# Optimization experiments

Hardware: AMD Instinct MI355X
Metric: run time of the kernel (lower is better)

## Reference

```python
import jax, jax.numpy as jnp
import numpy as np

H = 256   # hidden_size
D = 256   # embedding_dim
C = 111   # num_classes


def _pos_encoding(L, d):
    pos = jnp.arange(L, dtype=jnp.float32)[:, None]
    div = jnp.exp(jnp.arange(0, d, 2, dtype=jnp.float32) * (-np.log(10000.0) / d))
    pe = jnp.zeros((L, d), dtype=jnp.float32)
    pe = pe.at[:, 0::2].set(jnp.sin(pos * div))
    pe = pe.at[:, 1::2].set(jnp.cos(pos * div))
    return pe


def setup_inputs() -> dict:
    key = jax.random.key(0)
    ks = jax.random.split(key, 12)
    B, Cin, Hh, Ww, T = 64, 1024, 16, 64, 64
    s = 0.02
    return {
        "feature_map": jax.random.normal(ks[0], (B, Cin, Hh, Ww), jnp.float32),
        "count_vector": jax.random.uniform(ks[1], (B, C), jnp.float32),
        "target": jax.random.randint(ks[2], (B, T), 0, C),
        "conv_w": jax.random.normal(ks[3], (2 * H, Cin), jnp.float32) * s,
        "conv_b": jnp.zeros((2 * H,), jnp.float32),
        "emb": jax.random.normal(ks[4], (C, D), jnp.float32) * s,
        "gru_wih": jax.random.normal(ks[5], (3 * H, D + H + C), jnp.float32) * s,
        "gru_whh": jax.random.normal(ks[6], (3 * H, H), jnp.float32) * s,
        "gru_bih": jnp.zeros((3 * H,), jnp.float32),
        "gru_bhh": jnp.zeros((3 * H,), jnp.float32),
        "attn_w": jax.random.normal(ks[7], (H, 2 * H), jnp.float32) * s,
        "attn_b": jnp.zeros((H,), jnp.float32),
        "attn_v": jax.random.normal(ks[8], (1, H), jnp.float32) * s,
        "attn_vb": jnp.zeros((1,), jnp.float32),
        "cov_w": jax.random.normal(ks[9], (H, 1), jnp.float32) * s,
        "cov_b": jnp.zeros((H,), jnp.float32),
        "out_w": jax.random.normal(ks[10], (C, 2 * H + C), jnp.float32) * s,
        "out_b": jnp.zeros((C,), jnp.float32),
    }


def reference(feature_map, count_vector, target, conv_w, conv_b, emb,
              gru_wih, gru_whh, gru_bih, gru_bhh, attn_w, attn_b,
              attn_v, attn_vb, cov_w, cov_b, out_w, out_b):
    B, _, hh, ww = feature_map.shape
    L = hh * ww
    # 1x1 conv + permute to (B, h, w, 2H), add positional encoding, flatten
    feats = jnp.einsum('bchw,oc->bhwo', feature_map, conv_w) + conv_b
    pe = _pos_encoding(L, 2 * H).reshape(hh, ww, 2 * H)
    feats = (feats + pe[None]).reshape(B, L, 2 * H)
    # attention_w(projected_features) is time-invariant -> hoist out of the loop
    Wf = jnp.einsum('bld,hd->blh', feats, attn_w) + attn_b  # (B, L, H)

    # teacher forcing with ratio 1.0: inputs are <sos>=1 then target[:, :-1]
    y_in = jnp.concatenate([jnp.ones((B, 1), target.dtype), target[:, :-1]], axis=1)

    def gru_cell(x, h):  # PyTorch GRUCell math
        gi = x @ gru_wih.T + gru_bih
        gh = h @ gru_whh.T + gru_bhh
        i_r, i_z, i_n = jnp.split(gi, 3, axis=-1)
        h_r, h_z, h_n = jnp.split(gh, 3, axis=-1)
        r = jax.nn.sigmoid(i_r + h_r)
        z = jax.nn.sigmoid(i_z + h_z)
        n = jnp.tanh(i_n + r * h_n)
        return (1.0 - z) * n + z * h

    def step(carry, y_t):
        h, cov = carry  # h: (B,H), cov: (B,L)
        embedded = emb[y_t]
        a = jnp.tanh(Wf + cov[:, :, None] * cov_w[:, 0] + cov_b + h[:, None, :])
        scores = jnp.einsum('blh,h->bl', a, attn_v[0]) + attn_vb[0]
        alpha = jax.nn.softmax(scores, axis=1)
        cov = cov + alpha
        context = jnp.einsum('bl,bld->bd', alpha, feats)[:, :H]
        x = jnp.concatenate([embedded, context, count_vector], axis=1)
        h = gru_cell(x, h)
        out_t = jnp.concatenate([h, context, count_vector], axis=1) @ out_w.T + out_b
        return (h, cov), out_t

    h0 = jnp.zeros((B, H), feats.dtype)
    cov0 = jnp.zeros((B, L), feats.dtype)
    _, outs = jax.lax.scan(step, (h0, cov0), y_in.T)  # (T, B, C)
    return jnp.transpose(outs, (1, 0, 2))
```

## Files before the change

### kernel.cpp

```cpp
#include <hip/hip_runtime.h>
#include <hip/hip_bf16.h>
#include <cstdint>
#include <cstddef>

#define B_   64
#define CIN  1024
#define L_   1024
#define T_   64
#define Hh_  256
#define Dd_  256
#define Cc_  111
#define NO_  512
#define KX_  623

typedef __attribute__((ext_vector_type(8))) short short8;
typedef __attribute__((ext_vector_type(4))) float floatx4;

__device__ __forceinline__ float bf2f(unsigned short u) {
    union { unsigned int i; float f; } v; v.i = ((unsigned int)u) << 16; return v.f;
}
__device__ __forceinline__ unsigned short f2bf(float f) {
    union { float f; unsigned int i; } v; v.f = f;
    return (unsigned short)((v.i + 0x7fffu + ((v.i >> 16) & 1u)) >> 16);
}
__device__ __forceinline__ float frcp(float x) { return __builtin_amdgcn_rcpf(x); }
__device__ __forceinline__ float tanh_fast(float x) {
    return 1.0f - 2.0f * frcp(1.0f + __expf(2.0f * x));
}
__device__ __forceinline__ float sig_fast(float x) {
    return frcp(1.0f + __expf(-x));
}


__global__ void pe_kernel(float* __restrict__ PE) {
    int idx = blockIdx.x * 256 + threadIdx.x;
    if (idx >= L_ * NO_) return;
    int l = idx >> 9, j = idx & 511;
    int i2 = j & ~1;
    float div = expf((float)i2 * (-9.210340371976184f / 512.0f));
    float arg = (float)l * div;
    PE[idx] = (j & 1) ? cosf(arg) : sinf(arg);
}

__global__ void wc_kernel(const float* __restrict__ conv_w,
                          const float* __restrict__ attn_w,
                          unsigned short* __restrict__ Wc) {
    int c = blockIdx.x * 256 + threadIdx.x;
    int o = blockIdx.y;
    float v;
    if (o < 256) {
        v = conv_w[(size_t)o * CIN + c];
    } else {
        const float* aw = attn_w + (size_t)(o - 256) * 512;
        float a = 0.0f;
        for (int d = 0; d < 512; ++d)
            a = fmaf(aw[d], conv_w[(size_t)d * CIN + c], a);
        v = a;
    }
    Wc[(size_t)o * CIN + c] = f2bf(v);
}

__global__ void biasf_kernel(const float* __restrict__ conv_b,
                             const float* __restrict__ PE,
                             float* __restrict__ biasC) {
    int idx = blockIdx.x * 256 + threadIdx.x;
    int l = idx >> 8, j = idx & 255;
    biasC[(size_t)l * NO_ + j] = conv_b[j] + PE[(size_t)l * NO_ + j];
}

__global__ void biasw_kernel(const float* __restrict__ conv_b,
                             const float* __restrict__ PE,
                             const float* __restrict__ attn_w,
                             const float* __restrict__ attn_b,
                             float* __restrict__ biasC) {
    int l = blockIdx.x * 256 + threadIdx.x;
    int h = blockIdx.y;
    const float* aw = attn_w + (size_t)h * 512;
    const float* pe = PE + (size_t)l * NO_;
    float a = 0.0f;
    for (int d = 0; d < 512; ++d)
        a = fmaf(aw[d], conv_b[d] + pe[d], a);
    biasC[(size_t)l * NO_ + 256 + h] = a + attn_b[h];
}

__global__ void wiht_kernel(const float* __restrict__ wih, unsigned short* __restrict__ WihT) {
    int idx = blockIdx.x * 256 + threadIdx.x;
    if (idx >= 768 * KX_) return;
    int o = idx / KX_, k = idx - o * KX_;
    WihT[(size_t)k * 768 + o] = f2bf(wih[idx]);
}
__global__ void whht_kernel(const float* __restrict__ whh, unsigned short* __restrict__ WhhT) {
    int idx = blockIdx.x * 256 + threadIdx.x;
    if (idx >= 768 * 256) return;
    int o = idx >> 8, k = idx & 255;
    WhhT[(size_t)k * 768 + o] = f2bf(whh[idx]);
}
__global__ void woutt_kernel(const float* __restrict__ outw, unsigned short* __restrict__ WoutT) {
    int idx = blockIdx.x * 256 + threadIdx.x;
    if (idx >= Cc_ * KX_) return;
    int c = idx / KX_, k = idx - c * KX_;
    WoutT[(size_t)k * 128 + c] = f2bf(outw[idx]);
}

__global__ void zero_kernel(int* __restrict__ p, int n) {
    int i = blockIdx.x * 256 + threadIdx.x;
    if (i < n) p[i] = 0;
}

__global__ __launch_bounds__(256) void gemm_feats(
    const float* __restrict__ fm,
    const unsigned short* __restrict__ Wc,
    const float* __restrict__ biasC,
    unsigned short* __restrict__ F) {
    __shared__ __align__(16) unsigned short Als[128 * 40];
    __shared__ __align__(16) unsigned short Bls[128 * 40];
    const int tid  = threadIdx.x;
    const int bx   = blockIdx.x;
    const int bb   = bx >> 3;
    const int l0   = (bx & 7) << 7;
    const int n0   = blockIdx.y << 7;
    const int wid  = tid >> 6;
    const int lane = tid & 63;
    const int m0w  = (wid & 1) << 6;
    const int n0w  = (wid >> 1) << 6;
    const int quad = lane >> 4;
    const int l16  = lane & 15;

    floatx4 acc[4][4];
#pragma unroll
    for (int i = 0; i < 4; ++i)
#pragma unroll
        for (int j = 0; j < 4; ++j)
            acc[i][j] = (floatx4){0.f, 0.f, 0.f, 0.f};

    const int lt    = tid & 127;
    const int chalf = tid >> 7;
    const float* fmb = fm + ((size_t)bb * CIN) * L_ + l0 + lt;
    const int bo = tid >> 2;
    const int bc = (tid & 3) << 3;
    const int swzA = ((lt >> 2) & 3) << 3;

    for (int kk = 0; kk < 32; ++kk) {
        const int c0 = kk << 5;
        __syncthreads();
#pragma unroll
        for (int i = 0; i < 8; ++i) {
            int cc = (chalf + (i << 1)) << 1;
            float v0 = fmb[(size_t)(c0 + cc) * L_];
            float v1 = fmb[(size_t)(c0 + cc + 1) * L_];
            unsigned int pk = (unsigned int)f2bf(v0) | ((unsigned int)f2bf(v1) << 16);
            *(unsigned int*)(&Als[lt * 40 + (cc ^ swzA)]) = pk;
        }
#pragma unroll
        for (int i = 0; i < 2; ++i) {
            int o = bo + (i << 6);
            uint4 w = *(const uint4*)(&Wc[(size_t)(n0 + o) * CIN + c0 + bc]);
            *(uint4*)(&Bls[o * 40 + bc]) = w;
        }
        __syncthreads();
        short8 afr[4], bfr[4];
#pragma unroll
        for (int mf = 0; mf < 4; ++mf) {
            int mm = m0w + (mf << 4) + l16;
            int k0 = (quad << 3) ^ (((mm >> 2) & 3) << 3);
            afr[mf] = *(const short8*)(&Als[mm * 40 + k0]);
        }
#pragma unroll
        for (int nf = 0; nf < 4; ++nf) {
            int nn = n0w + (nf << 4) + l16;
            bfr[nf] = *(const short8*)(&Bls[nn * 40 + (quad << 3)]);
        }
#pragma unroll
        for (int mf = 0; mf < 4; ++mf)
#pragma unroll
            for (int nf = 0; nf < 4; ++nf)
                acc[mf][nf] = __builtin_amdgcn_mfma_f32_16x16x32_bf16(afr[mf], bfr[nf], acc[mf][nf], 0, 0, 0);
    }

#pragma unroll
    for (int mf = 0; mf < 4; ++mf) {
#pragma unroll
        for (int nf = 0; nf < 4; ++nf) {
            int colg = n0 + n0w + (nf << 4) + l16;
#pragma unroll
            for (int r = 0; r < 4; ++r) {
                int lb = l0 + m0w + (mf << 4) + (quad << 2) + r;
                float v = acc[mf][nf][r] + biasC[(size_t)lb * NO_ + colg];
                F[((size_t)bb * L_ + lb) * NO_ + colg] = f2bf(v);
            }
        }
    }
}


__device__ __forceinline__ void batch_barrier(int* bar, int target, int tid) {
    __syncthreads();
    if (tid == 0) {
        __hip_atomic_fetch_add(bar, 1, __ATOMIC_RELEASE, __HIP_MEMORY_SCOPE_AGENT);
        while (__hip_atomic_load(bar, __ATOMIC_RELAXED, __HIP_MEMORY_SCOPE_AGENT) < target) {
            __builtin_amdgcn_s_sleep(2);
        }
    }
    __syncthreads();
}

__global__ __launch_bounds__(1024, 4) void decoder_kernel(
    const unsigned short* __restrict__ F,
    const unsigned short* __restrict__ WihT,
    const unsigned short* __restrict__ WhhT,
    const unsigned short* __restrict__ WoutT,
    const float* __restrict__ cvv,
    const int* __restrict__ tgt,
    const float* __restrict__ emb,
    const float* __restrict__ bih,
    const float* __restrict__ bhh,
    const float* __restrict__ attn_v,
    const float* __restrict__ attn_vb,
    const float* __restrict__ cov_w,
    const float* __restrict__ cov_b,
    const float* __restrict__ outb,
    int* __restrict__ bar,
    float* __restrict__ gsum,
    float* __restrict__ gctx,
    float* __restrict__ ggih,
    float* __restrict__ OUT) {
    __shared__ __align__(16) unsigned short Wls[256 * 256];
    __shared__ float sc[256];
    __shared__ float cov[256];
    __shared__ float xv[640];
    __shared__ float xo[640];
    __shared__ float hv[256];
    __shared__ __align__(16) float hbs[256];
    __shared__ __align__(16) float cwls[256];
    __shared__ __align__(16) float avls[256];
    __shared__ float gi[768];
    __shared__ float gh[768];
    __shared__ float ctxp[2048];
    __shared__ float outp[1024];
    __shared__ float red[32];
    __shared__ int   tok[T_];

    const int tid  = threadIdx.x;
    const int bxr  = blockIdx.x;
    const int q_   = bxr >> 3;
    const int sub  = q_ & 3;
    const int b    = (bxr & 7) | ((q_ >> 2) << 3);
    const int l0   = sub << 8;
    const int lane = tid & 63;
    const int wid  = tid >> 6;
    const int l16  = tid & 15;
    const int lg   = tid >> 4;

    int* mybar = bar + b * 16;

    if (tid < 256) {
        cov[tid] = 0.0f; hv[tid] = 0.0f; hbs[tid] = cov_b[tid];
        cwls[tid] = cov_w[tid]; avls[tid] = attn_v[tid];
    }
    if (tid >= 512 && tid < 512 + Cc_) xv[tid] = cvv[b * Cc_ + (tid - 512)];
    if (tid >= KX_ && tid < 640) xo[tid] = 0.0f;
    if (tid < T_) tok[tid] = (tid == 0) ? 1 : tgt[b * T_ + tid - 1];

    const float avb = attn_vb[0];

#pragma unroll
    for (int i = 0; i < 8; ++i) {
        int c   = (i << 10) + tid;
        int row = c >> 5;
        int col = (c & 31) << 3;
        *(uint4*)(&Wls[(row << 8) + col]) =
            *(const uint4*)(F + (((size_t)(b * L_ + l0 + row)) << 9) + Hh_ + col);
    }

    unsigned int fctx[32];
    {
        const int hp = (tid & 127) << 1;
        const int ch = tid >> 7;
        const unsigned short* fb = F + (((size_t)(b * L_ + l0 + (ch << 5))) << 9) + hp;
#pragma unroll
        for (int i = 0; i < 32; ++i)
            fctx[i] = *(const unsigned int*)(fb + ((size_t)i << 9));
    }

    const int cbase = sub * 28;
    const int ccnt  = (sub == 3) ? 27 : 28;
    const int kg0 = sub * 156;
    const int kg1 = (kg0 + 156 > KX_) ? KX_ : kg0 + 156;
    const int kh0 = sub << 6;

    unsigned short wout_r[20];
    {
        int cc = tid & 31, ch = tid >> 5, k0 = ch * 20;
#pragma unroll
        for (int i = 0; i < 20; ++i) {
            int k = k0 + i;
            wout_r[i] = (k < KX_) ? WoutT[(size_t)k * 128 + cbase + cc] : (unsigned short)0;
        }
    }

    int nsync = 0;
    __syncthreads();

    float ecur = 0.0f;
    if (tid < 256) ecur = emb[(size_t)tok[0] * Dd_ + tid];

    for (int t = 0; t < T_; ++t) {
        const int par = t & 1;
        float* myctx = gctx + (((size_t)b * 2 + par) * 4) * 256;
        float* mysum = gsum + ((size_t)b * 2 + par) * 4;
        float* mygg  = ggih + (((size_t)b * 2 + par) * 4) * 1536;

        if (tid < 256) {
            xv[tid] = ecur;
            if (t + 1 < T_) ecur = emb[(size_t)tok[t + 1] * Dd_ + tid];
        }

#pragma unroll
        for (int pass = 0; pass < 4; ++pass) {
            int ll = (pass << 6) + lg;
            float covl = cov[ll];
            const unsigned short* wf = &Wls[ll << 8];
            float a = 0.0f;
#pragma unroll
            for (int j = 0; j < 4; ++j) {
                const int hb0 = (j << 6) + (l16 << 2);
                uint2 w = *(const uint2*)(wf + hb0);
                float4 cw4 = *(const float4*)(&cwls[hb0]);
                float4 av4 = *(const float4*)(&avls[hb0]);
                float4 hb4 = *(const float4*)(&hbs[hb0]);
                float g0 = bf2f((unsigned short)(w.x & 0xffffu)) + fmaf(covl, cw4.x, hb4.x);
                float g1 = bf2f((unsigned short)(w.x >> 16))     + fmaf(covl, cw4.y, hb4.y);
                float g2 = bf2f((unsigned short)(w.y & 0xffffu)) + fmaf(covl, cw4.z, hb4.z);
                float g3 = bf2f((unsigned short)(w.y >> 16))     + fmaf(covl, cw4.w, hb4.w);
                a = fmaf(av4.x, tanh_fast(g0), a);
                a = fmaf(av4.y, tanh_fast(g1), a);
                a = fmaf(av4.z, tanh_fast(g2), a);
                a = fmaf(av4.w, tanh_fast(g3), a);
            }
            a += __shfl_xor(a, 1);
            a += __shfl_xor(a, 2);
            a += __shfl_xor(a, 4);
            a += __shfl_xor(a, 8);
            if (l16 == 0) sc[ll] = __expf(a + avb);
        }
        __syncthreads();

        if (tid < 256) {
            float e = sc[tid];
#pragma unroll
            for (int off = 1; off < 64; off <<= 1) e += __shfl_xor(e, off);
            if (lane == 0) red[wid] = e;
        }

        {
            int hp = (tid & 127) << 1;
            int ch = tid >> 7;
            float c0a = 0.0f, c1a = 0.0f;
#pragma unroll
            for (int i = 0; i < 32; ++i) {
                float al = sc[(ch << 5) + i];
                unsigned int w = fctx[i];
                c0a = fmaf(al, bf2f((unsigned short)(w & 0xffffu)), c0a);
                c1a = fmaf(al, bf2f((unsigned short)(w >> 16)), c1a);
            }
            ctxp[(ch << 8) + hp]     = c0a;
            ctxp[(ch << 8) + hp + 1] = c1a;
        }
        __syncthreads();

        if (tid < 256) {
            float s2 = 0.0f;
#pragma unroll
            for (int i = 0; i < 8; ++i) s2 += ctxp[(i << 8) + tid];
            __hip_atomic_store(&myctx[sub * 256 + tid], s2, __ATOMIC_RELAXED, __HIP_MEMORY_SCOPE_AGENT);
        } else if (tid == 256) {
            float ss = red[0] + red[1] + red[2] + red[3];
            __hip_atomic_store(&mysum[sub], ss, __ATOMIC_RELAXED, __HIP_MEMORY_SCOPE_AGENT);
        }

        ++nsync;
        batch_barrier(mybar, 4 * nsync, tid);

        float s2 = 0.0f;
        if (tid < 256) {
#pragma unroll
            for (int s = 0; s < 4; ++s)
                s2 += __hip_atomic_load(&myctx[s * 256 + tid], __ATOMIC_RELAXED, __HIP_MEMORY_SCOPE_AGENT);
        } else if (tid == 256) {
            float S = 0.0f;
#pragma unroll
            for (int s = 0; s < 4; ++s)
                S += __hip_atomic_load(&mysum[s], __ATOMIC_RELAXED, __HIP_MEMORY_SCOPE_AGENT);
            red[16] = frcp(S);
        }
        __syncthreads();
        float rS = red[16];
        if (tid < 256) {
            xv[256 + tid] = s2 * rS;
            cov[tid] += sc[tid] * rS;
        }
        __syncthreads();

        if (tid < 384) {
            int o = tid << 1;
            float a0 = 0.0f, a1 = 0.0f;
            const unsigned short* wp = WihT + (size_t)kg0 * 768 + o;
#pragma unroll 4
            for (int k = kg0; k < kg1; ++k) {
                float x = xv[k];
                unsigned int w = *(const unsigned int*)wp;
                wp += 768;
                a0 = fmaf(x, bf2f((unsigned short)(w & 0xffffu)), a0);
                a1 = fmaf(x, bf2f((unsigned short)(w >> 16)), a1);
            }
            __hip_atomic_store(&mygg[sub * 1536 + o],     a0, __ATOMIC_RELAXED, __HIP_MEMORY_SCOPE_AGENT);
            __hip_atomic_store(&mygg[sub * 1536 + o + 1], a1, __ATOMIC_RELAXED, __HIP_MEMORY_SCOPE_AGENT);
        } else if (tid < 768) {
            int o = (tid - 384) << 1;
            float a0 = 0.0f, a1 = 0.0f;
            const unsigned short* wp = WhhT + (size_t)kh0 * 768 + o;
#pragma unroll 4
            for (int k = kh0; k < kh0 + 64; ++k) {
                float x = hv[k];
                unsigned int w = *(const unsigned int*)wp;
                wp += 768;
                a0 = fmaf(x, bf2f((unsigned short)(w & 0xffffu)), a0);
                a1 = fmaf(x, bf2f((unsigned short)(w >> 16)), a1);
            }
            __hip_atomic_store(&mygg[sub * 1536 + 768 + o],     a0, __ATOMIC_RELAXED, __HIP_MEMORY_SCOPE_AGENT);
            __hip_atomic_store(&mygg[sub * 1536 + 768 + o + 1], a1, __ATOMIC_RELAXED, __HIP_MEMORY_SCOPE_AGENT);
        }

        ++nsync;
        batch_barrier(mybar, 4 * nsync, tid);

        if (tid < 384) {
            int o = tid << 1;
            float v0 = bih[o], v1 = bih[o + 1];
#pragma unroll
            for (int s = 0; s < 4; ++s) {
                v0 += __hip_atomic_load(&mygg[s * 1536 + o],     __ATOMIC_RELAXED, __HIP_MEMORY_SCOPE_AGENT);
                v1 += __hip_atomic_load(&mygg[s * 1536 + o + 1], __ATOMIC_RELAXED, __HIP_MEMORY_SCOPE_AGENT);
            }
            gi[o] = v0; gi[o + 1] = v1;
        } else if (tid < 768) {
            int o = (tid - 384) << 1;
            float v0 = bhh[o], v1 = bhh[o + 1];
#pragma unroll
            for (int s = 0; s < 4; ++s) {
                v0 += __hip_atomic_load(&mygg[s * 1536 + 768 + o],     __ATOMIC_RELAXED, __HIP_MEMORY_SCOPE_AGENT);
                v1 += __hip_atomic_load(&mygg[s * 1536 + 768 + o + 1], __ATOMIC_RELAXED, __HIP_MEMORY_SCOPE_AGENT);
            }
            gh[o] = v0; gh[o + 1] = v1;
        }
        __syncthreads();

        if (tid < 256) {
            float r = sig_fast(gi[tid] + gh[tid]);
            float z = sig_fast(gi[256 + tid] + gh[256 + tid]);
            float n = tanh_fast(fmaf(r, gh[512 + tid], gi[512 + tid]));
            float hold = hv[tid];
            float hn = (1.0f - z) * n + z * hold;
            hv[tid] = hn;
            hbs[tid] = hn + cov_b[tid];
            xo[tid] = hn;
        } else if (tid < KX_) {
            xo[tid] = xv[tid];
        }
        __syncthreads();

        {
            int ch = tid >> 5;
            int k0 = ch * 20;
            float a = 0.0f;
#pragma unroll
            for (int i = 0; i < 20; ++i)
                a = fmaf(xo[k0 + i], bf2f(wout_r[i]), a);
            outp[tid] = a;
        }
        __syncthreads();
        if (tid < ccnt) {
            float s3 = outb[cbase + tid];
#pragma unroll
            for (int i = 0; i < 32; ++i) s3 += outp[(i << 5) + tid];
            __builtin_nontemporal_store(s3, &OUT[((size_t)b * T_ + t) * Cc_ + cbase + tid]);
        }
        __syncthreads();
    }
}

extern "C" void kernel_launch(void* const* d_in, const int* in_sizes, int n_in,
                              void* d_out, int out_size, void* d_ws, size_t ws_size,
                              hipStream_t stream) {
    const float* fm      = (const float*)d_in[0];
    const float* cvv     = (const float*)d_in[1];
    const int*   tgt     = (const int*)d_in[2];
    const float* conv_w  = (const float*)d_in[3];
    const float* conv_b  = (const float*)d_in[4];
    const float* emb     = (const float*)d_in[5];
    const float* wih     = (const float*)d_in[6];
    const float* whh     = (const float*)d_in[7];
    const float* bih     = (const float*)d_in[8];
    const float* bhh     = (const float*)d_in[9];
    const float* attn_w  = (const float*)d_in[10];
    const float* attn_b  = (const float*)d_in[11];
    const float* attn_v  = (const float*)d_in[12];
    const float* attn_vb = (const float*)d_in[13];
    const float* cov_w   = (const float*)d_in[14];
    const float* cov_b   = (const float*)d_in[15];
    const float* outw    = (const float*)d_in[16];
    const float* outb    = (const float*)d_in[17];
    float* OUT = (float*)d_out;
    char* ws = (char*)d_ws;

    unsigned short* F     = (unsigned short*)(ws);
    unsigned short* Wc    = (unsigned short*)(ws + 67108864);
    float*          biasC = (float*)(ws + 68157440);
    float*          PE    = (float*)(ws + 70254592);
    unsigned short* WihT  = (unsigned short*)(ws + 72351744);
    unsigned short* WhhT  = (unsigned short*)(ws + 73308672);
    unsigned short* WoutT = (unsigned short*)(ws + 73701888);

    int*   bar  = (int*)(ws + 68157440);
    float* gsum = (float*)(ws + 68161536);
    float* gctx = (float*)(ws + 68165632);
    float* ggih = (float*)(ws + 68689920);

    pe_kernel<<<2048, 256, 0, stream>>>(PE);
    wc_kernel<<<dim3(4, 512), 256, 0, stream>>>(conv_w, attn_w, Wc);
    biasf_kernel<<<1024, 256, 0, stream>>>(conv_b, PE, biasC);
    biasw_kernel<<<dim3(4, 256), 256, 0, stream>>>(conv_b, PE, attn_w, attn_b, biasC);
    wiht_kernel<<<1869, 256, 0, stream>>>(wih, WihT);
    whht_kernel<<<768, 256, 0, stream>>>(whh, WhhT);
    woutt_kernel<<<271, 256, 0, stream>>>(outw, WoutT);
    gemm_feats<<<dim3(512, 4), 256, 0, stream>>>(fm, Wc, biasC, F);
    zero_kernel<<<4, 256, 0, stream>>>(bar, 1024);
    decoder_kernel<<<256, 1024, 0, stream>>>(F, WihT, WhhT, WoutT,
        cvv, tgt, emb, bih, bhh, attn_v, attn_vb, cov_w, cov_b, outb,
        bar, gsum, gctx, ggih, OUT);
}
```

Measured before the change: 2.857 ms.

## Precompute embedding and count-vector GRU input terms, cut per-step barriers to one

Adds two setup kernels that compute the embedding-token and count-vector (plus bias) contributions to the GRU input gates once. Each block then multiplies only its unnormalized partial context by the context slice of W_ih, and the softmax normalization is applied after the cross-block reduction. This removes one of the two inter-block batch barriers per time step and a trailing __syncthreads. In exchange, each block now does the full 256-long W_hh matvec redundantly instead of a quarter of it.

Result: slower. 3.329 ms (+16.5%).

```diff
diff --git a/kernel.cpp b/kernel.cpp
--- a/kernel.cpp
+++ b/kernel.cpp
@@ -100,6 +100,49 @@
     if (idx >= Cc_ * KX_) return;
     int c = idx / KX_, k = idx - c * KX_;
     WoutT[(size_t)k * 128 + c] = f2bf(outw[idx]);
+}
+
+__global__ void gietok_kernel(const unsigned short* __restrict__ WihT,
+                              const float* __restrict__ emb,
+                              float* __restrict__ GIEt) {
+    int c = blockIdx.x;
+    int tid = threadIdx.x;
+    __shared__ float x[256];
+    x[tid] = emb[(size_t)c * Dd_ + tid];
+    __syncthreads();
+    float a0 = 0.0f, a1 = 0.0f, a2 = 0.0f;
+    for (int k = 0; k < 256; ++k) {
+        float xv = x[k];
+        const unsigned short* w = WihT + (size_t)k * 768;
+        a0 = fmaf(xv, bf2f(w[tid]), a0);
+        a1 = fmaf(xv, bf2f(w[256 + tid]), a1);
+        a2 = fmaf(xv, bf2f(w[512 + tid]), a2);
+    }
+    GIEt[(size_t)c * 768 + tid]       = a0;
+    GIEt[(size_t)c * 768 + 256 + tid] = a1;
+    GIEt[(size_t)c * 768 + 512 + tid] = a2;
+}
+
+__global__ void gicv_kernel(const unsigned short* __restrict__ WihT,
+                            const float* __restrict__ cvv,
+                            const float* __restrict__ bih,
+                            float* __restrict__ GICV) {
+    int b = blockIdx.x;
+    int tid = threadIdx.x;
+    __shared__ float x[112];
+    if (tid < Cc_) x[tid] = cvv[(size_t)b * Cc_ + tid];
+    __syncthreads();
+    float a0 = 0.0f, a1 = 0.0f, a2 = 0.0f;
+    for (int k = 0; k < Cc_; ++k) {
+        float xv = x[k];
+        const unsigned short* w = WihT + (size_t)(512 + k) * 768;
+        a0 = fmaf(xv, bf2f(w[tid]), a0);
+        a1 = fmaf(xv, bf2f(w[256 + tid]), a1);
+        a2 = fmaf(xv, bf2f(w[512 + tid]), a2);
+    }
+    GICV[(size_t)b * 768 + tid]       = a0 + bih[tid];
+    GICV[(size_t)b * 768 + 256 + tid] = a1 + bih[256 + tid];
+    GICV[(size_t)b * 768 + 512 + tid] = a2 + bih[512 + tid];
 }
 
 __global__ void zero_kernel(int* __restrict__ p, int n) {
@@ -211,8 +254,8 @@
     const unsigned short* __restrict__ WoutT,
     const float* __restrict__ cvv,
     const int* __restrict__ tgt,
-    const float* __restrict__ emb,
-    const float* __restrict__ bih,
+    const float* __restrict__ GIEt,
+    const float* __restrict__ GICV,
     const float* __restrict__ bhh,
     const float* __restrict__ attn_v,
     const float* __restrict__ attn_vb,
@@ -227,7 +270,7 @@
     __shared__ __align__(16) unsigned short Wls[256 * 256];
     __shared__ float sc[256];
     __shared__ float cov[256];
-    __shared__ float xv[640];
+    __shared__ float cs[256];
     __shared__ float xo[640];
     __shared__ float hv[256];
     __shared__ __align__(16) float hbs[256];
@@ -257,7 +300,7 @@
         cov[tid] = 0.0f; hv[tid] = 0.0f; hbs[tid] = cov_b[tid];
         cwls[tid] = cov_w[tid]; avls[tid] = attn_v[tid];
     }
-    if (tid >= 512 && tid < 512 + Cc_) xv[tid] = cvv[b * Cc_ + (tid - 512)];
+    if (tid >= 512 && tid < 512 + Cc_) xo[tid] = cvv[b * Cc_ + (tid - 512)];
     if (tid >= KX_ && tid < 640) xo[tid] = 0.0f;
     if (tid < T_) tok[tid] = (tid == 0) ? 1 : tgt[b * T_ + tid - 1];
 
@@ -284,9 +327,6 @@
 
     const int cbase = sub * 28;
     const int ccnt  = (sub == 3) ? 27 : 28;
-    const int kg0 = sub * 156;
-    const int kg1 = (kg0 + 156 > KX_) ? KX_ : kg0 + 156;
-    const int kh0 = sub << 6;
 
     unsigned short wout_r[20];
     {
@@ -298,22 +338,13 @@
         }
     }
 
-    int nsync = 0;
     __syncthreads();
-
-    float ecur = 0.0f;
-    if (tid < 256) ecur = emb[(size_t)tok[0] * Dd_ + tid];
 
     for (int t = 0; t < T_; ++t) {
         const int par = t & 1;
         float* myctx = gctx + (((size_t)b * 2 + par) * 4) * 256;
         float* mysum = gsum + ((size_t)b * 2 + par) * 4;
-        float* mygg  = ggih + (((size_t)b * 2 + par) * 4) * 1536;
-
-        if (tid < 256) {
-            xv[tid] = ecur;
-            if (t + 1 < T_) ecur = emb[(size_t)tok[t + 1] * Dd_ + tid];
-        }
+        float* mygg  = ggih + (((size_t)b * 2 + par) * 4) * 768;
 
 #pragma unroll
         for (int pass = 0; pass < 4; ++pass) {
@@ -372,86 +403,73 @@
             float s2 = 0.0f;
 #pragma unroll
             for (int i = 0; i < 8; ++i) s2 += ctxp[(i << 8) + tid];
+            cs[tid] = s2;
             __hip_atomic_store(&myctx[sub * 256 + tid], s2, __ATOMIC_RELAXED, __HIP_MEMORY_SCOPE_AGENT);
         } else if (tid == 256) {
             float ss = red[0] + red[1] + red[2] + red[3];
             __hip_atomic_store(&mysum[sub], ss, __ATOMIC_RELAXED, __HIP_MEMORY_SCOPE_AGENT);
         }
-
-        ++nsync;
-        batch_barrier(mybar, 4 * nsync, tid);
-
-        float s2 = 0.0f;
-        if (tid < 256) {
-#pragma unroll
-            for (int s = 0; s < 4; ++s)
-                s2 += __hip_atomic_load(&myctx[s * 256 + tid], __ATOMIC_RELAXED, __HIP_MEMORY_SCOPE_AGENT);
-        } else if (tid == 256) {
-            float S = 0.0f;
-#pragma unroll
-            for (int s = 0; s < 4; ++s)
-                S += __hip_atomic_load(&mysum[s], __ATOMIC_RELAXED, __HIP_MEMORY_SCOPE_AGENT);
-            red[16] = frcp(S);
-        }
-        __syncthreads();
-        float rS = red[16];
-        if (tid < 256) {
-            xv[256 + tid] = s2 * rS;
-            cov[tid] += sc[tid] * rS;
-        }
         __syncthreads();
 
         if (tid < 384) {
             int o = tid << 1;
             float a0 = 0.0f, a1 = 0.0f;
-            const unsigned short* wp = WihT + (size_t)kg0 * 768 + o;
+            const unsigned short* wp = WihT + (size_t)256 * 768 + o;
 #pragma unroll 4
-            for (int k = kg0; k < kg1; ++k) {
-                float x = xv[k];
+            for (int k = 0; k < 256; ++k) {
+                float x = cs[k];
                 unsigned int w = *(const unsigned int*)wp;
                 wp += 768;
                 a0 = fmaf(x, bf2f((unsigned short)(w & 0xffffu)), a0);
                 a1 = fmaf(x, bf2f((unsigned short)(w >> 16)), a1);
             }
-            __hip_atomic_store(&mygg[sub * 1536 + o],     a0, __ATOMIC_RELAXED, __HIP_MEMORY_SCOPE_AGENT);
-            __hip_atomic_store(&mygg[sub * 1536 + o + 1], a1, __ATOMIC_RELAXED, __HIP_MEMORY_SCOPE_AGENT);
+            __hip_atomic_store(&mygg[sub * 768 + o],     a0, __ATOMIC_RELAXED, __HIP_MEMORY_SCOPE_AGENT);
+            __hip_atomic_store(&mygg[sub * 768 + o + 1], a1, __ATOMIC_RELAXED, __HIP_MEMORY_SCOPE_AGENT);
         } else if (tid < 768) {
             int o = (tid - 384) << 1;
             float a0 = 0.0f, a1 = 0.0f;
-            const unsigned short* wp = WhhT + (size_t)kh0 * 768 + o;
+            const unsigned short* wp = WhhT + o;
 #pragma unroll 4
-            for (int k = kh0; k < kh0 + 64; ++k) {
+            for (int k = 0; k < 256; ++k) {
                 float x = hv[k];
                 unsigned int w = *(const unsigned int*)wp;
                 wp += 768;
                 a0 = fmaf(x, bf2f((unsigned short)(w & 0xffffu)), a0);
                 a1 = fmaf(x, bf2f((unsigned short)(w >> 16)), a1);
             }
-            __hip_atomic_store(&mygg[sub * 1536 + 768 + o],     a0, __ATOMIC_RELAXED, __HIP_MEMORY_SCOPE_AGENT);
-            __hip_atomic_store(&mygg[sub * 1536 + 768 + o + 1], a1, __ATOMIC_RELAXED, __HIP_MEMORY_SCOPE_AGENT);
-        }
-
-        ++nsync;
-        batch_barrier(mybar, 4 * nsync, tid);
-
-        if (tid < 384) {
-            int o = tid << 1;
-            float v0 = bih[o], v1 = bih[o + 1];
-#pragma unroll
-            for (int s = 0; s < 4; ++s) {
-                v0 += __hip_atomic_load(&mygg[s * 1536 + o],     __ATOMIC_RELAXED, __HIP_MEMORY_SCOPE_AGENT);
-                v1 += __hip_atomic_load(&mygg[s * 1536 + o + 1], __ATOMIC_RELAXED, __HIP_MEMORY_SCOPE_AGENT);
+            gh[o]     = a0 + bhh[o];
+            gh[o + 1] = a1 + bhh[o + 1];
+        }
+
+        batch_barrier(mybar, 4 * (t + 1), tid);
+
+        if (tid < 640) {
+            float S = 0.0f;
+#pragma unroll
+            for (int s = 0; s < 4; ++s)
+                S += __hip_atomic_load(&mysum[s], __ATOMIC_RELAXED, __HIP_MEMORY_SCOPE_AGENT);
+            float rS = frcp(S);
+            if (tid < 256) {
+                float s2 = 0.0f;
+#pragma unroll
+                for (int s = 0; s < 4; ++s)
+                    s2 += __hip_atomic_load(&myctx[s * 256 + tid], __ATOMIC_RELAXED, __HIP_MEMORY_SCOPE_AGENT);
+                xo[256 + tid] = s2 * rS;
+                cov[tid] += sc[tid] * rS;
+            } else {
+                int o = (tid - 256) << 1;
+                float sy0 = 0.0f, sy1 = 0.0f;
+#pragma unroll
+                for (int s = 0; s < 4; ++s) {
+                    sy0 += __hip_atomic_load(&mygg[s * 768 + o],     __ATOMIC_RELAXED, __HIP_MEMORY_SCOPE_AGENT);
+                    sy1 += __hip_atomic_load(&mygg[s * 768 + o + 1], __ATOMIC_RELAXED, __HIP_MEMORY_SCOPE_AGENT);
+                }
+                int tk = tok[t];
+                float2 ge = *(const float2*)(GIEt + (size_t)tk * 768 + o);
+                float2 gc = *(const float2*)(GICV + (size_t)b * 768 + o);
+                gi[o]     = ge.x + gc.x + rS * sy0;
+                gi[o + 1] = ge.y + gc.y + rS * sy1;
             }
-            gi[o] = v0; gi[o + 1] = v1;
-        } else if (tid < 768) {
-            int o = (tid - 384) << 1;
-            float v0 = bhh[o], v1 = bhh[o + 1];
-#pragma unroll
-            for (int s = 0; s < 4; ++s) {
-                v0 += __hip_atomic_load(&mygg[s * 1536 + 768 + o],     __ATOMIC_RELAXED, __HIP_MEMORY_SCOPE_AGENT);
-                v1 += __hip_atomic_load(&mygg[s * 1536 + 768 + o + 1], __ATOMIC_RELAXED, __HIP_MEMORY_SCOPE_AGENT);
-            }
-            gh[o] = v0; gh[o + 1] = v1;
         }
         __syncthreads();
 
@@ -464,8 +482,6 @@
             hv[tid] = hn;
             hbs[tid] = hn + cov_b[tid];
             xo[tid] = hn;
-        } else if (tid < KX_) {
-            xo[tid] = xv[tid];
         }
         __syncthreads();
 
@@ -485,7 +501,6 @@
             for (int i = 0; i < 32; ++i) s3 += outp[(i << 5) + tid];
             __builtin_nontemporal_store(s3, &OUT[((size_t)b * T_ + t) * Cc_ + cbase + tid]);
         }
-        __syncthreads();
     }
 }
 
@@ -525,6 +540,8 @@
     float* gsum = (float*)(ws + 68161536);
     float* gctx = (float*)(ws + 68165632);
     float* ggih = (float*)(ws + 68689920);
+    float* GIEt = (float*)(ws + 70262784);
+    float* GICV = (float*)(ws + 70603776);
 
     pe_kernel<<<2048, 256, 0, stream>>>(PE);
     wc_kernel<<<dim3(4, 512), 256, 0, stream>>>(conv_w, attn_w, Wc);
@@ -533,9 +550,11 @@
     wiht_kernel<<<1869, 256, 0, stream>>>(wih, WihT);
     whht_kernel<<<768, 256, 0, stream>>>(whh, WhhT);
     woutt_kernel<<<271, 256, 0, stream>>>(outw, WoutT);
+    gietok_kernel<<<Cc_, 256, 0, stream>>>(WihT, emb, GIEt);
+    gicv_kernel<<<B_, 256, 0, stream>>>(WihT, cvv, bih, GICV);
     gemm_feats<<<dim3(512, 4), 256, 0, stream>>>(fm, Wc, biasC, F);
     zero_kernel<<<4, 256, 0, stream>>>(bar, 1024);
     decoder_kernel<<<256, 1024, 0, stream>>>(F, WihT, WhhT, WoutT,
-        cvv, tgt, emb, bih, bhh, attn_v, attn_vb, cov_w, cov_b, outb,
+        cvv, tgt, GIEt, GICV, bhh, attn_v, attn_vb, cov_w, cov_b, outb,
         bar, gsum, gctx, ggih, OUT);
 }
```
